# Performance work log

Hardware: AMD Instinct MI355X
Metric: run time of the kernel (lower is better)

## Reference

```python
import jax, jax.numpy as jnp
import numpy as np

MASK_VAL = -10000.0
HEADS = 16

def setup_inputs() -> dict:
    key = jax.random.key(0)
    ks = jax.random.split(key, 4)
    dim = 1024
    x = jax.random.normal(ks[0], (4, 2048, dim), dtype=jnp.float32)
    Wq = jax.random.normal(ks[1], (dim, dim), dtype=jnp.float32) * (dim ** -0.5)
    Wkv = jax.random.normal(ks[2], (dim, 2 * dim), dtype=jnp.float32) * (dim ** -0.5)
    Wout = jax.random.normal(ks[3], (dim, dim), dtype=jnp.float32) * (dim ** -0.5)
    bout = jnp.zeros((dim,), dtype=jnp.float32)
    return {"x": x, "Wq": Wq, "Wkv": Wkv, "Wout": Wout, "bout": bout}

def reference(x, Wq, Wkv, Wout, bout):
    b, n, dim = x.shape
    h = HEADS
    d = dim // h
    scale = dim ** -0.5  # NOTE: module scales by full dim, not head dim
    q = x @ Wq                       # [b,n,dim]
    kv = x @ Wkv                     # [b,n,2*dim]
    k, v = jnp.split(kv, 2, axis=-1)
    split = lambda t: t.reshape(b, n, h, d).transpose(0, 2, 1, 3)  # b h n d
    q, k, v = split(q), split(k), split(v)
    dots = jnp.einsum('bhid,bhjd->bhij', q, k) * scale
    causal = jnp.triu(jnp.ones((n, n), dtype=bool), 1)
    dots = jnp.where(causal, MASK_VAL, dots)
    attn = jax.nn.softmax(dots, axis=-1)
    out = jnp.einsum('bhij,bhjd->bhid', attn, v)
    out = out.transpose(0, 2, 1, 3).reshape(b, n, dim)
    return out @ Wout + bout
```

## Files before the change

### kernel.cpp

```cpp
#include <hip/hip_runtime.h>

typedef unsigned short u16;
typedef __attribute__((ext_vector_type(4))) float f32x4;
typedef __attribute__((ext_vector_type(8))) short bf16x8;
typedef __attribute__((ext_vector_type(4))) short s16x4;

#define MFMA_BF16(a, b, c) __builtin_amdgcn_mfma_f32_16x16x32_bf16((a), (b), (c), 0, 0, 0)

#if defined(__has_builtin)
#if __has_builtin(__builtin_amdgcn_mfma_f32_16x16x16bf16_1k)
#define HAVE_MFMA16 1
#define MFMA16(a, b, c) __builtin_amdgcn_mfma_f32_16x16x16bf16_1k((a), (b), (c), 0, 0, 0)
#endif
#endif
#ifndef HAVE_MFMA16
#define HAVE_MFMA16 0
#endif

static constexpr int kDim   = 1024;
static constexpr int kSeq   = 2048;
static constexpr int kBatch = 4;
static constexpr int kHeads = 16;
static constexpr int kTok   = kBatch * kSeq;
static constexpr int kQKV   = 3 * kDim;
static constexpr float kQscale = 0.045084220027780106f;

__device__ __forceinline__ u16 f2bf(float f) {
  unsigned int u = __float_as_uint(f);
  u += 0x7fffu + ((u >> 16) & 1u);
  return (u16)(u >> 16);
}

__device__ __forceinline__ float fast_exp2(float x) {
#if __has_builtin(__builtin_amdgcn_exp2f)
  return __builtin_amdgcn_exp2f(x);
#else
  return exp2f(x);
#endif
}

__device__ __forceinline__ unsigned pack_bf16(float lo, float hi) {
  const unsigned ulo = __float_as_uint(lo) + 0x8000u;
  const unsigned uhi = __float_as_uint(hi) + 0x8000u;
#if __has_builtin(__builtin_amdgcn_perm)
  return __builtin_amdgcn_perm(uhi, ulo, 0x07060302u);
#else
  return (uhi & 0xFFFF0000u) | (ulo >> 16);
#endif
}

__device__ __forceinline__ void gl_lds16(const void* g, void* l) {
  __builtin_amdgcn_global_load_lds(
      (const __attribute__((address_space(1))) void*)g,
      (__attribute__((address_space(3))) void*)l, 16, 0, 0);
}

__global__ __launch_bounds__(256) void cvt_f32_to_bf16(const float* __restrict__ in,
                                                       u16* __restrict__ out, int n8) {
  int i = blockIdx.x * 256 + threadIdx.x;
  if (i >= n8) return;
  const float4* p = (const float4*)in + (size_t)i * 2;
  float4 a = p[0], b = p[1];
  alignas(16) u16 o[8];
  o[0] = f2bf(a.x); o[1] = f2bf(a.y); o[2] = f2bf(a.z); o[3] = f2bf(a.w);
  o[4] = f2bf(b.x); o[5] = f2bf(b.y); o[6] = f2bf(b.z); o[7] = f2bf(b.w);
  *(uint4*)(out + (size_t)i * 8) = *(const uint4*)o;
}

__global__ __launch_bounds__(256) void transpose_cvt(const float* __restrict__ src,
                                                     u16* __restrict__ dst, int R, int C) {
  __shared__ u16 tile[64][65];
  const int r0 = blockIdx.y * 64, c0 = blockIdx.x * 64;
  const int t = threadIdx.x;
#pragma unroll
  for (int i = 0; i < 16; ++i) {
    const int idx = i * 256 + t;
    const int rr = idx >> 6, cc = idx & 63;
    tile[rr][cc] = f2bf(src[(size_t)(r0 + rr) * C + c0 + cc]);
  }
  __syncthreads();
#pragma unroll
  for (int i = 0; i < 16; ++i) {
    const int idx = i * 256 + t;
    const int rr = idx >> 6, cc = idx & 63;
    dst[(size_t)(c0 + rr) * R + r0 + cc] = tile[cc][rr];
  }
}

__global__ __launch_bounds__(256) void transpose_v(const u16* __restrict__ QKV,
                                                   u16* __restrict__ Vt) {
  __shared__ u16 tile[64][65];
  const int n0 = blockIdx.x * 64;
  const int bh = blockIdx.y;
  const int b = bh >> 4, h = bh & 15;
  const int t = threadIdx.x;
#pragma unroll
  for (int i = 0; i < 16; ++i) {
    const int idx = i * 256 + t;
    const int nn = idx >> 6, dd = idx & 63;
    tile[nn][dd] = QKV[(size_t)(b * kSeq + n0 + nn) * kQKV + 2048 + h * 64 + dd];
  }
  __syncthreads();
#pragma unroll
  for (int i = 0; i < 16; ++i) {
    const int idx = i * 256 + t;
    const int dd = idx >> 6, nn = idx & 63;
    Vt[((size_t)bh * 64 + dd) * kSeq + n0 + nn] = tile[nn][dd];
  }
}

template <int OUT_F32>
__global__ __launch_bounds__(256) void gemm_bt(const u16* __restrict__ A,
                                               const u16* __restrict__ Bt,
                                               void* __restrict__ Cout,
                                               const float* __restrict__ bias,
                                               int M, int N, int K,
                                               int qcols, float qs) {
  __shared__ u16 As[128 * 64];
  __shared__ u16 Bs[128 * 64];
  const int t = threadIdx.x;
  const int l = t & 63, w = t >> 6;
  const int g = l >> 4, r = l & 15;

  const int gx = gridDim.x;
  int wg = blockIdx.y * gx + blockIdx.x;
  const int chunk = (gx * gridDim.y) >> 3;
  wg = (wg & 7) * chunk + (wg >> 3);
  const int m0 = (wg / gx) * 128, n0 = (wg % gx) * 128;
  const int wr = (w >> 1) * 64, wc = (w & 1) * 64;

  f32x4 acc[4][4];
#pragma unroll
  for (int m = 0; m < 4; ++m)
#pragma unroll
    for (int n = 0; n < 4; ++n) acc[m][n] = f32x4{0.f, 0.f, 0.f, 0.f};

  const int srow = t >> 3;
  const int sgran = t & 7;
  const int scol = (sgran ^ (srow & 7)) * 8;
  const u16* ga = A + (size_t)(m0 + srow) * K + scol;
  const u16* gb = Bt + (size_t)(n0 + srow) * K + scol;
  char* lA = (char*)As + t * 16;
  char* lB = (char*)Bs + t * 16;
  const int rsw = r & 7;

  for (int k0 = 0; k0 < K; k0 += 64) {
#pragma unroll
    for (int i = 0; i < 4; ++i) {
      gl_lds16(ga + k0 + (size_t)(i * 32) * K, lA + i * 4096);
      gl_lds16(gb + k0 + (size_t)(i * 32) * K, lB + i * 4096);
    }
    __syncthreads();
#pragma unroll
    for (int kk = 0; kk < 2; ++kk) {
      bf16x8 af[4], bfr[4];
#pragma unroll
      for (int m = 0; m < 4; ++m)
        af[m] = *(const bf16x8*)(As + (wr + m * 16 + r) * 64 + (((kk * 4 + g) ^ rsw) * 8));
#pragma unroll
      for (int n = 0; n < 4; ++n)
        bfr[n] = *(const bf16x8*)(Bs + (wc + n * 16 + r) * 64 + (((kk * 4 + g) ^ rsw) * 8));
#pragma unroll
      for (int m = 0; m < 4; ++m)
#pragma unroll
        for (int n = 0; n < 4; ++n)
          acc[m][n] = MFMA_BF16(af[m], bfr[n], acc[m][n]);
    }
    __syncthreads();
  }

#pragma unroll
  for (int m = 0; m < 4; ++m)
#pragma unroll
    for (int n = 0; n < 4; ++n)
#pragma unroll
      for (int j = 0; j < 4; ++j) {
        const int row = m0 + wr + m * 16 + g * 4 + j;
        const int col = n0 + wc + n * 16 + r;
        if (OUT_F32) {
          ((float*)Cout)[(size_t)row * N + col] = acc[m][n][j] + bias[col];
        } else {
          float v = acc[m][n][j];
          if (col < qcols) v *= qs;
          ((u16*)Cout)[(size_t)row * N + col] = f2bf(v);
        }
      }
}

__global__ __launch_bounds__(512, 4) void attn_fwd(const u16* __restrict__ QKV,
                                                   const u16* __restrict__ Vt,
                                                   u16* __restrict__ Ob) {
  __shared__ u16 Kl[2][64 * 64];
  __shared__ u16 Vl[2][64 * 64];
  int wg = blockIdx.y * 8 + blockIdx.x;
  wg = (wg & 7) * 64 + (wg >> 3);
  const int ib = wg & 7;
  const int bh = wg >> 3;
  const int b = bh >> 4, h = bh & 15;
  const int t = threadIdx.x;
  const int w = t >> 6;
  const int l = t & 63;
  const int g = l >> 4;
  const int qr = l & 15;
  const int sw = qr & 7;
  const int srow = t >> 3;
  const int sgran = t & 7;
  const int sg_off = (sgran ^ (srow & 7)) * 8;

  const u16* kbase = QKV + (size_t)b * kSeq * kQKV + 1024 + h * 64 + (size_t)srow * kQKV + sg_off;
  const u16* vbase = Vt + ((size_t)bh * 64 + srow) * kSeq + sg_off;

  for (int pass = 0; pass < 2; ++pass) {
    const int qblk = pass ? (15 - ib) : ib;
    const int q0 = qblk * 128;
    const int qrow_g = q0 + w * 16 + qr;

    const u16* qptr = QKV + (size_t)(b * kSeq + qrow_g) * kQKV + h * 64 + g * 8;
    bf16x8 qf[2];
    qf[0] = *(const bf16x8*)qptr;
    qf[1] = *(const bf16x8*)(qptr + 32);

    f32x4 oacc[4];
#pragma unroll
    for (int d = 0; d < 4; ++d) oacc[d] = f32x4{0.f, 0.f, 0.f, 0.f};
    float lsum = 0.f;

    const int nkv = 2 * qblk + 2;

    gl_lds16(kbase, (char*)Kl[0] + t * 16);
    gl_lds16(vbase, (char*)Vl[0] + t * 16);

    for (int kb = 0; kb < nkv; ++kb) {
      const int cur = kb & 1;
      if (kb + 1 < nkv) {
        const int kv1 = (kb + 1) * 64;
        gl_lds16(kbase + (size_t)kv1 * kQKV, (char*)Kl[cur ^ 1] + t * 16);
        gl_lds16(vbase + kv1, (char*)Vl[cur ^ 1] + t * 16);
        asm volatile("s_waitcnt vmcnt(2)" ::: "memory");
      } else {
        asm volatile("s_waitcnt vmcnt(0)" ::: "memory");
      }
      __builtin_amdgcn_s_barrier();
      __builtin_amdgcn_sched_barrier(0);

      const u16* Kc = Kl[cur];
      const u16* Vc = Vl[cur];
      const int kv0 = kb * 64;
      const bool any_valid = kv0 <= q0 + w * 16 + 15;
      const bool need_mask = kv0 + 63 > q0 + w * 16;

      if (any_valid) {
        f32x4 sacc[4];
#pragma unroll
        for (int n = 0; n < 4; ++n) sacc[n] = f32x4{0.f, 0.f, 0.f, 0.f};
        __builtin_amdgcn_s_setprio(1);
#pragma unroll
        for (int n = 0; n < 4; ++n)
#pragma unroll
          for (int c = 0; c < 2; ++c) {
            bf16x8 kf = *(const bf16x8*)(Kc + (n * 16 + qr) * 64 + ((c * 4 + g) ^ sw) * 8);
            sacc[n] = MFMA_BF16(kf, qf[c], sacc[n]);
          }
        __builtin_amdgcn_s_setprio(0);

        float s2[16];
#pragma unroll
        for (int n = 0; n < 4; ++n)
#pragma unroll
          for (int j = 0; j < 4; ++j) s2[n * 4 + j] = sacc[n][j];
        if (need_mask) {
#pragma unroll
          for (int n = 0; n < 4; ++n)
#pragma unroll
            for (int j = 0; j < 4; ++j) {
              const int kv = kv0 + n * 16 + g * 4 + j;
              if (kv > qrow_g) s2[n * 4 + j] = -30000.0f;
            }
        }

        unsigned pk[4][2];
#pragma unroll
        for (int n = 0; n < 4; ++n)
#pragma unroll
          for (int hw = 0; hw < 2; ++hw) {
            const float p0 = fast_exp2(fminf(s2[n * 4 + hw * 2], 60.f));
            const float p1 = fast_exp2(fminf(s2[n * 4 + hw * 2 + 1], 60.f));
            lsum += p0 + p1;
            pk[n][hw] = pack_bf16(p0, p1);
          }

#if HAVE_MFMA16
        __builtin_amdgcn_s_setprio(1);
#pragma unroll
        for (int n = 0; n < 4; ++n) {
          union { unsigned u[2]; s16x4 v; } pa;
          pa.u[0] = pk[n][0];
          pa.u[1] = pk[n][1];
#pragma unroll
          for (int d = 0; d < 4; ++d) {
            const s16x4 vb = *(const s16x4*)(Vc + (d * 16 + qr) * 64 +
                                             (((2 * n + (g >> 1)) ^ sw) << 3) +
                                             ((g & 1) << 2));
            oacc[d] = MFMA16(pa.v, vb, oacc[d]);
          }
        }
        __builtin_amdgcn_s_setprio(0);
#else
        const int src0 = qr | (((g << 1) & 3) << 4);
        const int src1 = qr | ((((g << 1) + 1) & 3) << 4);
        const bool hi = (g >> 1) != 0;
#pragma unroll
        for (int c = 0; c < 2; ++c) {
          const unsigned a0 = __shfl(pk[2 * c][0], src0);
          const unsigned a1 = __shfl(pk[2 * c][1], src0);
          const unsigned a2 = __shfl(pk[2 * c + 1][0], src0);
          const unsigned a3 = __shfl(pk[2 * c + 1][1], src0);
          const unsigned b0 = __shfl(pk[2 * c][0], src1);
          const unsigned b1 = __shfl(pk[2 * c][1], src1);
          const unsigned b2 = __shfl(pk[2 * c + 1][0], src1);
          const unsigned b3 = __shfl(pk[2 * c + 1][1], src1);
          union { unsigned u[4]; bf16x8 v; } af;
          af.u[0] = hi ? a2 : a0;
          af.u[1] = hi ? a3 : a1;
          af.u[2] = hi ? b2 : b0;
          af.u[3] = hi ? b3 : b1;
          __builtin_amdgcn_s_setprio(1);
#pragma unroll
          for (int d = 0; d < 4; ++d) {
            bf16x8 vf = *(const bf16x8*)(Vc + (d * 16 + qr) * 64 + ((c * 4 + g) ^ sw) * 8);
            oacc[d] = MFMA_BF16(af.v, vf, oacc[d]);
          }
          __builtin_amdgcn_s_setprio(0);
        }
#endif
      }
      __builtin_amdgcn_s_barrier();
    }

    lsum += __shfl_xor(lsum, 16);
    lsum += __shfl_xor(lsum, 32);
    const float invl = 1.0f / lsum;
    float ir[4];
#pragma unroll
    for (int j = 0; j < 4; ++j) ir[j] = __shfl(invl, (l & 48) | (g * 4 + j));
#pragma unroll
    for (int d = 0; d < 4; ++d)
#pragma unroll
      for (int j = 0; j < 4; ++j) {
        const int row = q0 + w * 16 + g * 4 + j;
        const int col = h * 64 + d * 16 + qr;
        Ob[(size_t)(b * kSeq + row) * kDim + col] = f2bf(oacc[d][j] * ir[j]);
      }
  }
}

extern "C" void kernel_launch(void* const* d_in, const int* in_sizes, int n_in,
                              void* d_out, int out_size, void* d_ws, size_t ws_size,
                              hipStream_t stream) {
  const float* x    = (const float*)d_in[0];
  const float* Wq   = (const float*)d_in[1];
  const float* Wkv  = (const float*)d_in[2];
  const float* Wout = (const float*)d_in[3];
  const float* bout = (const float*)d_in[4];
  float* out = (float*)d_out;

  char* p = (char*)d_ws;
  u16* xb    = (u16*)p; p += (size_t)kTok * kDim * 2;
  u16* Wqkvt = (u16*)p; p += (size_t)kQKV * kDim * 2;
  u16* Wot   = (u16*)p; p += (size_t)kDim * kDim * 2;
  u16* QKV   = (u16*)p; p += (size_t)kTok * kQKV * 2;
  u16* Vt    = (u16*)p; p += (size_t)64 * 64 * kSeq * 2;
  u16* Ob    = (u16*)p; p += (size_t)kTok * kDim * 2;

  const int n8 = kTok * kDim / 8;
  cvt_f32_to_bf16<<<dim3((n8 + 255) / 256), 256, 0, stream>>>(x, xb, n8);
  transpose_cvt<<<dim3(kDim / 64, kDim / 64), 256, 0, stream>>>(Wq, Wqkvt, kDim, kDim);
  transpose_cvt<<<dim3(2 * kDim / 64, kDim / 64), 256, 0, stream>>>(
      Wkv, Wqkvt + (size_t)kDim * kDim, kDim, 2 * kDim);
  transpose_cvt<<<dim3(kDim / 64, kDim / 64), 256, 0, stream>>>(Wout, Wot, kDim, kDim);

  gemm_bt<0><<<dim3(kQKV / 128, kTok / 128), 256, 0, stream>>>(
      xb, Wqkvt, QKV, nullptr, kTok, kQKV, kDim, kDim, kQscale);
  transpose_v<<<dim3(kSeq / 64, kBatch * kHeads), 256, 0, stream>>>(QKV, Vt);
  attn_fwd<<<dim3(kSeq / 256, kBatch * kHeads), 512, 0, stream>>>(QKV, Vt, Ob);
  gemm_bt<1><<<dim3(kDim / 128, kTok / 128), 256, 0, stream>>>(
      Ob, Wot, out, bout, kTok, kDim, kDim, 0, 1.0f);
}
```

Measured before the change: 261.2 us.

## Give each attention wave two Q row tiles and merge prep kernels into one

The attention kernel now runs 4 waves of 256 threads, each owning 32 query rows (two 16-row tiles), instead of 8 waves owning 16 rows each. Every K/V fragment read from LDS is therefore reused across two MFMAs, and each thread issues two async loads per K/V tile. Separately, the x conversion and three weight transpose kernels are fused into a single launch that dispatches on block index. The attention change raises register pressure and lowers the number of waves per block, which can reduce latency hiding.

Result: slower. 273.5 us (+4.7%).

```diff
diff --git a/kernel.cpp b/kernel.cpp
--- a/kernel.cpp
+++ b/kernel.cpp
@@ -55,23 +55,33 @@
       (__attribute__((address_space(3))) void*)l, 16, 0, 0);
 }
 
-__global__ __launch_bounds__(256) void cvt_f32_to_bf16(const float* __restrict__ in,
-                                                       u16* __restrict__ out, int n8) {
-  int i = blockIdx.x * 256 + threadIdx.x;
-  if (i >= n8) return;
-  const float4* p = (const float4*)in + (size_t)i * 2;
-  float4 a = p[0], b = p[1];
-  alignas(16) u16 o[8];
-  o[0] = f2bf(a.x); o[1] = f2bf(a.y); o[2] = f2bf(a.z); o[3] = f2bf(a.w);
-  o[4] = f2bf(b.x); o[5] = f2bf(b.y); o[6] = f2bf(b.z); o[7] = f2bf(b.w);
-  *(uint4*)(out + (size_t)i * 8) = *(const uint4*)o;
-}
-
-__global__ __launch_bounds__(256) void transpose_cvt(const float* __restrict__ src,
-                                                     u16* __restrict__ dst, int R, int C) {
+__global__ __launch_bounds__(256) void prep(const float* __restrict__ x,
+                                            const float* __restrict__ Wq,
+                                            const float* __restrict__ Wkv,
+                                            const float* __restrict__ Wout,
+                                            u16* __restrict__ xb,
+                                            u16* __restrict__ Wqkvt,
+                                            u16* __restrict__ Wot) {
+  const int bid = blockIdx.x;
+  const int t = threadIdx.x;
+  if (bid < 4096) {
+    const int i = bid * 256 + t;
+    const float4* p = (const float4*)x + (size_t)i * 2;
+    float4 a = p[0], c = p[1];
+    alignas(16) u16 o[8];
+    o[0] = f2bf(a.x); o[1] = f2bf(a.y); o[2] = f2bf(a.z); o[3] = f2bf(a.w);
+    o[4] = f2bf(c.x); o[5] = f2bf(c.y); o[6] = f2bf(c.z); o[7] = f2bf(c.w);
+    *(uint4*)(xb + (size_t)i * 8) = *(const uint4*)o;
+    return;
+  }
   __shared__ u16 tile[64][65];
-  const int r0 = blockIdx.y * 64, c0 = blockIdx.x * 64;
-  const int t = threadIdx.x;
+  const float* src;
+  u16* dst;
+  int C, bx, by;
+  if (bid < 4352)      { const int id = bid - 4096; src = Wq;   dst = Wqkvt;                          C = kDim;     bx = id & 15; by = id >> 4; }
+  else if (bid < 4864) { const int id = bid - 4352; src = Wkv;  dst = Wqkvt + (size_t)kDim * kDim;    C = 2 * kDim; bx = id & 31; by = id >> 5; }
+  else                 { const int id = bid - 4864; src = Wout; dst = Wot;                            C = kDim;     bx = id & 15; by = id >> 4; }
+  const int r0 = by * 64, c0 = bx * 64;
 #pragma unroll
   for (int i = 0; i < 16; ++i) {
     const int idx = i * 256 + t;
@@ -83,7 +93,7 @@
   for (int i = 0; i < 16; ++i) {
     const int idx = i * 256 + t;
     const int rr = idx >> 6, cc = idx & 63;
-    dst[(size_t)(c0 + rr) * R + r0 + cc] = tile[cc][rr];
+    dst[(size_t)(c0 + rr) * kDim + r0 + cc] = tile[cc][rr];
   }
 }
 
@@ -187,7 +197,7 @@
       }
 }
 
-__global__ __launch_bounds__(512, 4) void attn_fwd(const u16* __restrict__ QKV,
+__global__ __launch_bounds__(256, 2) void attn_fwd(const u16* __restrict__ QKV,
                                                    const u16* __restrict__ Vt,
                                                    u16* __restrict__ Ob) {
   __shared__ u16 Kl[2][64 * 64];
@@ -213,30 +223,41 @@
   for (int pass = 0; pass < 2; ++pass) {
     const int qblk = pass ? (15 - ib) : ib;
     const int q0 = qblk * 128;
-    const int qrow_g = q0 + w * 16 + qr;
-
-    const u16* qptr = QKV + (size_t)(b * kSeq + qrow_g) * kQKV + h * 64 + g * 8;
-    bf16x8 qf[2];
-    qf[0] = *(const bf16x8*)qptr;
-    qf[1] = *(const bf16x8*)(qptr + 32);
-
-    f32x4 oacc[4];
-#pragma unroll
-    for (int d = 0; d < 4; ++d) oacc[d] = f32x4{0.f, 0.f, 0.f, 0.f};
-    float lsum = 0.f;
+    const int wrow = q0 + w * 32;
+    const int qrow0 = wrow + qr;
+    const int qrow1 = wrow + 16 + qr;
+
+    bf16x8 qf[2][2];
+#pragma unroll
+    for (int u = 0; u < 2; ++u) {
+      const u16* qptr = QKV + (size_t)(b * kSeq + wrow + u * 16 + qr) * kQKV + h * 64 + g * 8;
+      qf[u][0] = *(const bf16x8*)qptr;
+      qf[u][1] = *(const bf16x8*)(qptr + 32);
+    }
+
+    f32x4 oacc[2][4];
+#pragma unroll
+    for (int u = 0; u < 2; ++u)
+#pragma unroll
+      for (int d = 0; d < 4; ++d) oacc[u][d] = f32x4{0.f, 0.f, 0.f, 0.f};
+    float lsum0 = 0.f, lsum1 = 0.f;
 
     const int nkv = 2 * qblk + 2;
 
     gl_lds16(kbase, (char*)Kl[0] + t * 16);
+    gl_lds16(kbase + (size_t)32 * kQKV, (char*)Kl[0] + 4096 + t * 16);
     gl_lds16(vbase, (char*)Vl[0] + t * 16);
+    gl_lds16(vbase + (size_t)32 * kSeq, (char*)Vl[0] + 4096 + t * 16);
 
     for (int kb = 0; kb < nkv; ++kb) {
       const int cur = kb & 1;
       if (kb + 1 < nkv) {
         const int kv1 = (kb + 1) * 64;
         gl_lds16(kbase + (size_t)kv1 * kQKV, (char*)Kl[cur ^ 1] + t * 16);
+        gl_lds16(kbase + (size_t)(kv1 + 32) * kQKV, (char*)Kl[cur ^ 1] + 4096 + t * 16);
         gl_lds16(vbase + kv1, (char*)Vl[cur ^ 1] + t * 16);
-        asm volatile("s_waitcnt vmcnt(2)" ::: "memory");
+        gl_lds16(vbase + (size_t)32 * kSeq + kv1, (char*)Vl[cur ^ 1] + 4096 + t * 16);
+        asm volatile("s_waitcnt vmcnt(4)" ::: "memory");
       } else {
         asm volatile("s_waitcnt vmcnt(0)" ::: "memory");
       }
@@ -246,62 +267,62 @@
       const u16* Kc = Kl[cur];
       const u16* Vc = Vl[cur];
       const int kv0 = kb * 64;
-      const bool any_valid = kv0 <= q0 + w * 16 + 15;
-      const bool need_mask = kv0 + 63 > q0 + w * 16;
+      const bool any_valid = kv0 <= wrow + 31;
+      const bool need_mask = kv0 + 63 > wrow;
 
       if (any_valid) {
-        f32x4 sacc[4];
-#pragma unroll
-        for (int n = 0; n < 4; ++n) sacc[n] = f32x4{0.f, 0.f, 0.f, 0.f};
+        f32x4 sacc[2][4];
+#pragma unroll
+        for (int u = 0; u < 2; ++u)
+#pragma unroll
+          for (int n = 0; n < 4; ++n) sacc[u][n] = f32x4{0.f, 0.f, 0.f, 0.f};
         __builtin_amdgcn_s_setprio(1);
 #pragma unroll
         for (int n = 0; n < 4; ++n)
 #pragma unroll
           for (int c = 0; c < 2; ++c) {
             bf16x8 kf = *(const bf16x8*)(Kc + (n * 16 + qr) * 64 + ((c * 4 + g) ^ sw) * 8);
-            sacc[n] = MFMA_BF16(kf, qf[c], sacc[n]);
+            sacc[0][n] = MFMA_BF16(kf, qf[0][c], sacc[0][n]);
+            sacc[1][n] = MFMA_BF16(kf, qf[1][c], sacc[1][n]);
           }
         __builtin_amdgcn_s_setprio(0);
 
-        float s2[16];
+        unsigned pk[2][4][2];
 #pragma unroll
         for (int n = 0; n < 4; ++n)
 #pragma unroll
-          for (int j = 0; j < 4; ++j) s2[n * 4 + j] = sacc[n][j];
-        if (need_mask) {
-#pragma unroll
-          for (int n = 0; n < 4; ++n)
-#pragma unroll
-            for (int j = 0; j < 4; ++j) {
-              const int kv = kv0 + n * 16 + g * 4 + j;
-              if (kv > qrow_g) s2[n * 4 + j] = -30000.0f;
+          for (int hw = 0; hw < 2; ++hw) {
+            const int kvb = kv0 + n * 16 + g * 4 + hw * 2;
+#pragma unroll
+            for (int u = 0; u < 2; ++u) {
+              const int qrow_u = u ? qrow1 : qrow0;
+              float s0 = sacc[u][n][hw * 2];
+              float s1 = sacc[u][n][hw * 2 + 1];
+              if (need_mask) {
+                if (kvb > qrow_u) s0 = -30000.0f;
+                if (kvb + 1 > qrow_u) s1 = -30000.0f;
+              }
+              const float p0 = fast_exp2(fminf(s0, 60.f));
+              const float p1 = fast_exp2(fminf(s1, 60.f));
+              if (u) lsum1 += p0 + p1; else lsum0 += p0 + p1;
+              pk[u][n][hw] = pack_bf16(p0, p1);
             }
-        }
-
-        unsigned pk[4][2];
-#pragma unroll
-        for (int n = 0; n < 4; ++n)
-#pragma unroll
-          for (int hw = 0; hw < 2; ++hw) {
-            const float p0 = fast_exp2(fminf(s2[n * 4 + hw * 2], 60.f));
-            const float p1 = fast_exp2(fminf(s2[n * 4 + hw * 2 + 1], 60.f));
-            lsum += p0 + p1;
-            pk[n][hw] = pack_bf16(p0, p1);
           }
 
 #if HAVE_MFMA16
         __builtin_amdgcn_s_setprio(1);
 #pragma unroll
         for (int n = 0; n < 4; ++n) {
-          union { unsigned u[2]; s16x4 v; } pa;
-          pa.u[0] = pk[n][0];
-          pa.u[1] = pk[n][1];
+          union { unsigned uu[2]; s16x4 v; } pa0, pa1;
+          pa0.uu[0] = pk[0][n][0]; pa0.uu[1] = pk[0][n][1];
+          pa1.uu[0] = pk[1][n][0]; pa1.uu[1] = pk[1][n][1];
 #pragma unroll
           for (int d = 0; d < 4; ++d) {
             const s16x4 vb = *(const s16x4*)(Vc + (d * 16 + qr) * 64 +
                                              (((2 * n + (g >> 1)) ^ sw) << 3) +
                                              ((g & 1) << 2));
-            oacc[d] = MFMA16(pa.v, vb, oacc[d]);
+            oacc[0][d] = MFMA16(pa0.v, vb, oacc[0][d]);
+            oacc[1][d] = MFMA16(pa1.v, vb, oacc[1][d]);
           }
         }
         __builtin_amdgcn_s_setprio(0);
@@ -310,47 +331,51 @@
         const int src1 = qr | ((((g << 1) + 1) & 3) << 4);
         const bool hi = (g >> 1) != 0;
 #pragma unroll
-        for (int c = 0; c < 2; ++c) {
-          const unsigned a0 = __shfl(pk[2 * c][0], src0);
-          const unsigned a1 = __shfl(pk[2 * c][1], src0);
-          const unsigned a2 = __shfl(pk[2 * c + 1][0], src0);
-          const unsigned a3 = __shfl(pk[2 * c + 1][1], src0);
-          const unsigned b0 = __shfl(pk[2 * c][0], src1);
-          const unsigned b1 = __shfl(pk[2 * c][1], src1);
-          const unsigned b2 = __shfl(pk[2 * c + 1][0], src1);
-          const unsigned b3 = __shfl(pk[2 * c + 1][1], src1);
-          union { unsigned u[4]; bf16x8 v; } af;
-          af.u[0] = hi ? a2 : a0;
-          af.u[1] = hi ? a3 : a1;
-          af.u[2] = hi ? b2 : b0;
-          af.u[3] = hi ? b3 : b1;
-          __builtin_amdgcn_s_setprio(1);
-#pragma unroll
-          for (int d = 0; d < 4; ++d) {
-            bf16x8 vf = *(const bf16x8*)(Vc + (d * 16 + qr) * 64 + ((c * 4 + g) ^ sw) * 8);
-            oacc[d] = MFMA_BF16(af.v, vf, oacc[d]);
+        for (int u = 0; u < 2; ++u)
+#pragma unroll
+          for (int c = 0; c < 2; ++c) {
+            const unsigned a0 = __shfl(pk[u][2 * c][0], src0);
+            const unsigned a1 = __shfl(pk[u][2 * c][1], src0);
+            const unsigned a2 = __shfl(pk[u][2 * c + 1][0], src0);
+            const unsigned a3 = __shfl(pk[u][2 * c + 1][1], src0);
+            const unsigned b0 = __shfl(pk[u][2 * c][0], src1);
+            const unsigned b1 = __shfl(pk[u][2 * c][1], src1);
+            const unsigned b2 = __shfl(pk[u][2 * c + 1][0], src1);
+            const unsigned b3 = __shfl(pk[u][2 * c + 1][1], src1);
+            union { unsigned uu[4]; bf16x8 v; } af;
+            af.uu[0] = hi ? a2 : a0;
+            af.uu[1] = hi ? a3 : a1;
+            af.uu[2] = hi ? b2 : b0;
+            af.uu[3] = hi ? b3 : b1;
+#pragma unroll
+            for (int d = 0; d < 4; ++d) {
+              bf16x8 vf = *(const bf16x8*)(Vc + (d * 16 + qr) * 64 + ((c * 4 + g) ^ sw) * 8);
+              oacc[u][d] = MFMA_BF16(af.v, vf, oacc[u][d]);
+            }
           }
-          __builtin_amdgcn_s_setprio(0);
-        }
 #endif
       }
       __builtin_amdgcn_s_barrier();
     }
 
-    lsum += __shfl_xor(lsum, 16);
-    lsum += __shfl_xor(lsum, 32);
-    const float invl = 1.0f / lsum;
-    float ir[4];
-#pragma unroll
-    for (int j = 0; j < 4; ++j) ir[j] = __shfl(invl, (l & 48) | (g * 4 + j));
-#pragma unroll
-    for (int d = 0; d < 4; ++d)
-#pragma unroll
-      for (int j = 0; j < 4; ++j) {
-        const int row = q0 + w * 16 + g * 4 + j;
-        const int col = h * 64 + d * 16 + qr;
-        Ob[(size_t)(b * kSeq + row) * kDim + col] = f2bf(oacc[d][j] * ir[j]);
-      }
+#pragma unroll
+    for (int u = 0; u < 2; ++u) {
+      float ls = u ? lsum1 : lsum0;
+      ls += __shfl_xor(ls, 16);
+      ls += __shfl_xor(ls, 32);
+      const float invl = 1.0f / ls;
+      float ir[4];
+#pragma unroll
+      for (int j = 0; j < 4; ++j) ir[j] = __shfl(invl, (l & 48) | (g * 4 + j));
+#pragma unroll
+      for (int d = 0; d < 4; ++d)
+#pragma unroll
+        for (int j = 0; j < 4; ++j) {
+          const int row = wrow + u * 16 + g * 4 + j;
+          const int col = h * 64 + d * 16 + qr;
+          Ob[(size_t)(b * kSeq + row) * kDim + col] = f2bf(oacc[u][d][j] * ir[j]);
+        }
+    }
   }
 }
 
@@ -372,17 +397,12 @@
   u16* Vt    = (u16*)p; p += (size_t)64 * 64 * kSeq * 2;
   u16* Ob    = (u16*)p; p += (size_t)kTok * kDim * 2;
 
-  const int n8 = kTok * kDim / 8;
-  cvt_f32_to_bf16<<<dim3((n8 + 255) / 256), 256, 0, stream>>>(x, xb, n8);
-  transpose_cvt<<<dim3(kDim / 64, kDim / 64), 256, 0, stream>>>(Wq, Wqkvt, kDim, kDim);
-  transpose_cvt<<<dim3(2 * kDim / 64, kDim / 64), 256, 0, stream>>>(
-      Wkv, Wqkvt + (size_t)kDim * kDim, kDim, 2 * kDim);
-  transpose_cvt<<<dim3(kDim / 64, kDim / 64), 256, 0, stream>>>(Wout, Wot, kDim, kDim);
+  prep<<<dim3(5120), 256, 0, stream>>>(x, Wq, Wkv, Wout, xb, Wqkvt, Wot);
 
   gemm_bt<0><<<dim3(kQKV / 128, kTok / 128), 256, 0, stream>>>(
       xb, Wqkvt, QKV, nullptr, kTok, kQKV, kDim, kDim, kQscale);
   transpose_v<<<dim3(kSeq / 64, kBatch * kHeads), 256, 0, stream>>>(QKV, Vt);
-  attn_fwd<<<dim3(kSeq / 256, kBatch * kHeads), 512, 0, stream>>>(QKV, Vt, Ob);
+  attn_fwd<<<dim3(kSeq / 256, kBatch * kHeads), 256, 0, stream>>>(QKV, Vt, Ob);
   gemm_bt<1><<<dim3(kDim / 128, kTok / 128), 256, 0, stream>>>(
       Ob, Wot, out, bout, kTok, kDim, kDim, 0, 1.0f);
 }
```
